# Performance work log

Measured on AMD Instinct MI355X. Metric: run time of the kernel, lower is better.

The kernel has to match this reference:

```python
import jax, jax.numpy as jnp
import numpy as np

D_MODEL = 1024
N_HEADS = 16
D_HEAD = D_MODEL // N_HEADS
B, L = 4, 2048
NEG_INF = float('-inf')


def setup_inputs() -> dict:
    key = jax.random.key(0)
    ks = jax.random.split(key, 8)
    x = jax.random.normal(ks[0], (B, L, D_MODEL), dtype=jnp.float32)
    # sorted cumulative event times in hours (~0-2000h span)
    timestamps = jnp.cumsum(jax.random.uniform(ks[1], (B, L), dtype=jnp.float32), axis=-1)
    mask = jnp.ones((B, L), dtype=jnp.float32)
    s = 1.0 / np.sqrt(D_MODEL)
    W_qkv = jax.random.normal(ks[2], (3 * D_MODEL, D_MODEL), dtype=jnp.float32) * s
    b_qkv = jnp.zeros((3 * D_MODEL,), dtype=jnp.float32)
    W_out = jax.random.normal(ks[3], (D_MODEL, D_MODEL), dtype=jnp.float32) * s
    b_out = jnp.zeros((D_MODEL,), dtype=jnp.float32)
    decay_rate = jnp.full((N_HEADS,), 0.01, dtype=jnp.float32)
    return {"x": x, "timestamps": timestamps, "mask": mask,
            "W_qkv": W_qkv, "b_qkv": b_qkv, "W_out": W_out, "b_out": b_out,
            "decay_rate": decay_rate}


def reference(x, timestamps, mask, W_qkv, b_qkv, W_out, b_out, decay_rate):
    Bb, Ll, Dd = x.shape
    H, dh = N_HEADS, D_HEAD
    scale = dh ** (-0.5)
    qkv = x @ W_qkv.T + b_qkv                     # (B,L,3D)
    qkv = qkv.reshape(Bb, Ll, 3, H, dh).transpose(2, 0, 3, 1, 4)  # (3,B,H,L,dh)
    q, k, v = qkv[0], qkv[1], qkv[2]
    attn = jnp.einsum('bhqd,bhkd->bhqk', q, k) * scale
    t_diff = jnp.abs(timestamps[:, :, None] - timestamps[:, None, :])[:, None]  # (B,1,L,L)
    decay = jax.nn.softplus(decay_rate)[None, :, None, None]                    # (1,H,1,1)
    attn = attn - decay * t_diff / 24.0
    causal = jnp.triu(jnp.ones((Ll, Ll), dtype=bool), k=1)        # (L,L) True above diag
    attn = jnp.where(causal[None, None], NEG_INF, attn)
    pad = (mask == 0.0)[:, None, None, :]                         # (B,1,1,L) True=pad key
    attn = jnp.where(pad, NEG_INF, attn)
    attn = jax.nn.softmax(attn, axis=-1)
    out = jnp.einsum('bhqk,bhkd->bhqd', attn, v)                  # (B,H,L,dh)
    out = out.transpose(0, 2, 1, 3).reshape(Bb, Ll, Dd)
    return out @ W_out.T + b_out
```

## Files before the change

kernel.cpp:

```cpp
#include <hip/hip_runtime.h>
#include <stdint.h>
#include <math.h>

#define B_   4
#define L_   2048
#define H_   16
#define DH_  64
#define DM_  1024

typedef __bf16 bf16;
typedef __attribute__((ext_vector_type(8))) __bf16 bf16x8;
typedef __attribute__((ext_vector_type(4))) float f32x4;
typedef __attribute__((ext_vector_type(4))) int i32x4;
typedef __attribute__((ext_vector_type(4))) short s16x4;
typedef unsigned short u16;
typedef unsigned int u32;
typedef __attribute__((ext_vector_type(2))) unsigned int u32x2;
typedef __attribute__((ext_vector_type(4))) unsigned short u16x4;

typedef unsigned int u32g __attribute__((address_space(1)));
typedef unsigned int u32l __attribute__((address_space(3)));

__device__ __forceinline__ u16 f2bf(float f) {
  return __builtin_bit_cast(u16, (bf16)f);
}

__device__ __forceinline__ float exp2_fast(float x) {
  float r; asm("v_exp_f32 %0, %1" : "=v"(r) : "v"(x)); return r;
}

__device__ __forceinline__ void gload16(const void* g, void* l) {
  __builtin_amdgcn_global_load_lds((const u32g*)g, (u32l*)l, 16, 0, 0);
}

__device__ __forceinline__ f32x4 mfma16(s16x4 a, s16x4 b, f32x4 c) {
#if __has_builtin(__builtin_amdgcn_mfma_f32_16x16x16bf16_1k)
  return __builtin_amdgcn_mfma_f32_16x16x16bf16_1k(a, b, c, 0, 0, 0);
#else
  asm volatile("v_mfma_f32_16x16x16_bf16 %0, %1, %2, %0\n\ts_nop 7\n\ts_nop 2"
               : "+v"(c) : "v"(a), "v"(b));
  return c;
#endif
}

#define NX4 2097152
#define NQ4 786432
#define NO4 262144
#define NTOT4 (NX4 + NQ4 + NO4)
__global__ __launch_bounds__(256) void cvt3b(const float* __restrict__ x,
                                             const float* __restrict__ wq,
                                             const float* __restrict__ wo,
                                             u16* __restrict__ xb, u16* __restrict__ wqb,
                                             u16* __restrict__ wob,
                                             const float* __restrict__ ts,
                                             const float* __restrict__ msk,
                                             const float* __restrict__ decay,
                                             float* __restrict__ Bk) {
  int i = blockIdx.x * 256 + threadIdx.x;
  if (i >= NTOT4) {
    int j = i - NTOT4;
    int bh = j >> 11, l = j & (L_ - 1);
    int b = bh >> 4, h = bh & 15;
    float dc24 = log1pf(__expf(decay[h])) * (1.0f / 24.0f) * 1.44269504f;
    float tv = ts[b * L_ + l], mv = msk[b * L_ + l];
    Bk[j] = (mv != 0.f) ? dc24 * tv : -INFINITY;
    return;
  }
  const float* src; u16* dst; int j;
  if (i < NX4)            { src = x;  dst = xb;  j = i; }
  else if (i < NX4 + NQ4) { src = wq; dst = wqb; j = i - NX4; }
  else                    { src = wo; dst = wob; j = i - NX4 - NQ4; }
  f32x4 v = ((const f32x4*)src)[j];
  u16x4 o;
  o[0] = f2bf(v[0]); o[1] = f2bf(v[1]); o[2] = f2bf(v[2]); o[3] = f2bf(v[3]);
  ((u16x4*)dst)[j] = o;
}

__global__ __launch_bounds__(512) void gemm_qkv(
    const u16* __restrict__ A, const u16* __restrict__ Bm, const float* __restrict__ bias,
    u16* __restrict__ Qb, u16* __restrict__ Kb, u16* __restrict__ Vt)
{
  __shared__ char smem[135168];
  u16* ltr = (u16*)smem;
  const int K = 1024, nk = 16;

  const int tid = threadIdx.x;
  const int nwg = gridDim.x;
  int idx = blockIdx.x;
  idx = (idx & 7) * (nwg >> 3) + (idx >> 3);
  const int nbx = 12;
  const int bx = idx % nbx, by = idx / nbx;
  const int m0 = by << 8, n0 = bx << 8;

  const int lane = tid & 63, w = tid >> 6;
  const int g = lane >> 4, col = lane & 15;
  const int wr = w >> 2, wc = w & 3;

  f32x4 acc[8][4];
#pragma unroll
  for (int mt = 0; mt < 8; ++mt)
#pragma unroll
    for (int nt = 0; nt < 4; ++nt) {
      acc[mt][nt][0] = 0.f; acc[mt][nt][1] = 0.f;
      acc[mt][nt][2] = 0.f; acc[mt][nt][3] = 0.f;
    }

  auto SA = [&](int kt, int nb, int q) {
    char* dA = smem + (nb << 16);
    int c = (q << 9) + tid;
    int row = c >> 3, cc = c & 7;
    gload16(A + (size_t)(m0 + row) * K + (kt << 6) + ((cc ^ (row & 7)) << 3), dA + c * 16);
  };
  auto SB = [&](int kt, int nb, int q) {
    char* dB = smem + (nb << 16) + 32768;
    int c = (q << 9) + tid;
    int row = c >> 3, cc = c & 7;
    gload16(Bm + (size_t)(n0 + row) * K + (kt << 6) + ((cc ^ (row & 7)) << 3), dB + c * 16);
  };

  SA(0, 0, 0); SA(0, 0, 1); SA(0, 0, 2); SA(0, 0, 3);
  SB(0, 0, 0); SB(0, 0, 1); SB(0, 0, 2); SB(0, 0, 3);
  SA(1, 1, 0); SA(1, 1, 2); SB(1, 1, 0); SB(1, 1, 1); SA(1, 1, 1); SA(1, 1, 3);
  asm volatile("s_waitcnt vmcnt(6)" ::: "memory");
  __builtin_amdgcn_s_barrier();

  for (int t = 0; t < nk; ++t) {
    const char* bufA = smem + ((t & 1) << 16);
    const char* bufB = bufA + 32768;
    const int nbN = (t + 1) & 1;

    auto RDA = [&](int mt, int kk) {
      int row = wr * 128 + mt * 16 + col;
      return *(const bf16x8*)(bufA + row * 128 + ((((kk << 2) + g) ^ (row & 7)) << 4));
    };
    auto RDB = [&](int nt, int kk) {
      int row = wc * 64 + nt * 16 + col;
      return *(const bf16x8*)(bufB + row * 128 + ((((kk << 2) + g) ^ (row & 7)) << 4));
    };

    bf16x8 af[4][2], bfr[4][2];

#pragma unroll
    for (int mi = 0; mi < 4; ++mi) { af[mi][0] = RDA(mi, 0); af[mi][1] = RDA(mi, 1); }
#pragma unroll
    for (int ni = 0; ni < 2; ++ni) { bfr[ni][0] = RDB(ni, 0); bfr[ni][1] = RDB(ni, 1); }
    if (t + 1 < nk) { SB(t + 1, nbN, 2); SB(t + 1, nbN, 3); }
    __builtin_amdgcn_s_barrier();
    asm volatile("s_waitcnt lgkmcnt(0)" ::: "memory");
    __builtin_amdgcn_sched_barrier(0);
    __builtin_amdgcn_s_setprio(1);
#pragma unroll
    for (int mi = 0; mi < 4; ++mi)
#pragma unroll
      for (int ni = 0; ni < 2; ++ni)
#pragma unroll
        for (int kk = 0; kk < 2; ++kk)
          acc[mi][ni] = __builtin_amdgcn_mfma_f32_16x16x32_bf16(af[mi][kk], bfr[ni][kk], acc[mi][ni], 0, 0, 0);
    __builtin_amdgcn_s_setprio(0);
    __builtin_amdgcn_s_barrier();

#pragma unroll
    for (int ni = 2; ni < 4; ++ni) { bfr[ni][0] = RDB(ni, 0); bfr[ni][1] = RDB(ni, 1); }
    if (t + 2 < nk) { SA(t + 2, t & 1, 0); SA(t + 2, t & 1, 2); }
    __builtin_amdgcn_s_barrier();
    asm volatile("s_waitcnt lgkmcnt(0)" ::: "memory");
    __builtin_amdgcn_sched_barrier(0);
    __builtin_amdgcn_s_setprio(1);
#pragma unroll
    for (int mi = 0; mi < 4; ++mi)
#pragma unroll
      for (int ni = 2; ni < 4; ++ni)
#pragma unroll
        for (int kk = 0; kk < 2; ++kk)
          acc[mi][ni] = __builtin_amdgcn_mfma_f32_16x16x32_bf16(af[mi][kk], bfr[ni][kk], acc[mi][ni], 0, 0, 0);
    __builtin_amdgcn_s_setprio(0);
    __builtin_amdgcn_s_barrier();

#pragma unroll
    for (int mi = 0; mi < 4; ++mi) { af[mi][0] = RDA(mi + 4, 0); af[mi][1] = RDA(mi + 4, 1); }
    if (t + 2 < nk) { SB(t + 2, t & 1, 0); SB(t + 2, t & 1, 1); }
    __builtin_amdgcn_s_barrier();
    asm volatile("s_waitcnt lgkmcnt(0)" ::: "memory");
    __builtin_amdgcn_sched_barrier(0);
    __builtin_amdgcn_s_setprio(1);
#pragma unroll
    for (int mi = 0; mi < 4; ++mi)
#pragma unroll
      for (int ni = 2; ni < 4; ++ni)
#pragma unroll
        for (int kk = 0; kk < 2; ++kk)
          acc[mi + 4][ni] = __builtin_amdgcn_mfma_f32_16x16x32_bf16(af[mi][kk], bfr[ni][kk], acc[mi + 4][ni], 0, 0, 0);
    __builtin_amdgcn_s_setprio(0);
    __builtin_amdgcn_s_barrier();

    if (t + 2 < nk) { SA(t + 2, t & 1, 1); SA(t + 2, t & 1, 3); }
    __builtin_amdgcn_s_setprio(1);
#pragma unroll
    for (int mi = 0; mi < 4; ++mi)
#pragma unroll
      for (int ni = 0; ni < 2; ++ni)
#pragma unroll
        for (int kk = 0; kk < 2; ++kk)
          acc[mi + 4][ni] = __builtin_amdgcn_mfma_f32_16x16x32_bf16(af[mi][kk], bfr[ni][kk], acc[mi + 4][ni], 0, 0, 0);
    __builtin_amdgcn_s_setprio(0);
    if (t + 2 < nk) asm volatile("s_waitcnt vmcnt(6)" ::: "memory");
    else            asm volatile("s_waitcnt vmcnt(0)" ::: "memory");
    __builtin_amdgcn_s_barrier();
  }

  const int type = n0 >> 10;
  const float qsc = (type == 0) ? 0.125f * 1.44269504f : 1.0f;
#pragma unroll
  for (int nt = 0; nt < 4; ++nt) {
    int nn = wc * 64 + nt * 16 + col;
    float bv = bias[n0 + nn];
#pragma unroll
    for (int mt = 0; mt < 8; ++mt) {
      int mm = wr * 128 + mt * 16 + g * 4;
#pragma unroll
      for (int r = 0; r < 4; ++r) {
        u16 hv = f2bf((acc[mt][nt][r] + bv) * qsc);
        if (type < 2) ltr[(mm + r) * 264 + nn] = hv;
        else          ltr[nn * 264 + (mm + r)] = hv;
      }
    }
  }
  __syncthreads();
  if (type < 2) {
#pragma unroll
    for (int it = 0; it < 16; ++it) {
      int cid = tid + it * 512;
      int rrow = cid >> 5, cc = cid & 31;
      i32x4 v = *(const i32x4*)((const char*)ltr + rrow * 528 + cc * 16);
      int token = m0 + rrow;
      int bb = token >> 11, ll = token & (L_ - 1);
      int gn = n0 + cc * 8;
      int head = (gn & 1023) >> 6, d = gn & 63;
      u16* dst = (type == 0) ? Qb : Kb;
      *(i32x4*)(dst + ((size_t)((bb * H_ + head) * L_ + ll)) * 64 + d) = v;
    }
  } else {
#pragma unroll
    for (int it = 0; it < 16; ++it) {
      int cid = tid + it * 512;
      int rrow = cid >> 5, cc = cid & 31;
      i32x4 v = *(const i32x4*)((const char*)ltr + rrow * 528 + cc * 16);
      int gn = n0 + rrow;
      int head = (gn & 1023) >> 6, d = gn & 63;
      int token0 = m0 + cc * 8;
      int bb = token0 >> 11, ll = token0 & (L_ - 1);
      *(i32x4*)(Vt + ((size_t)((bb * H_ + head) * DH_ + d)) * L_ + ll) = v;
    }
  }
}

__global__ __launch_bounds__(512) void gemm_bf16(
    const u16* __restrict__ A, const u16* __restrict__ Bm, const float* __restrict__ bias,
    int M, int N, int K, int mode,
    u16* __restrict__ Qb, u16* __restrict__ Kb, u16* __restrict__ Vt, float* __restrict__ Cout)
{
  __shared__ char smem[147456];
  const int tid = threadIdx.x;
  const int nwg = gridDim.x;
  int idx = blockIdx.x;
  idx = (idx & 7) * (nwg >> 3) + (idx >> 3);
  const int nbx = N >> 7;
  const int bx = idx % nbx, by = idx / nbx;
  const int m0 = by << 8, n0 = bx << 7;

  const int lane = tid & 63, w = tid >> 6;
  const int g = lane >> 4, col = lane & 15;
  const int wr = w >> 1, wc = w & 1;

  f32x4 acc[4][4];
#pragma unroll
  for (int mt = 0; mt < 4; ++mt)
#pragma unroll
    for (int nt = 0; nt < 4; ++nt) {
      acc[mt][nt][0] = 0.f; acc[mt][nt][1] = 0.f;
      acc[mt][nt][2] = 0.f; acc[mt][nt][3] = 0.f;
    }

  auto STAGE_A = [&](int kt, int nb, int hh) {
    char* dA = smem + nb * 49152;
    const int k0 = kt << 6;
#pragma unroll
    for (int pp = hh * 2; pp < hh * 2 + 2; ++pp) {
      int c = tid + pp * 512;
      int row = c >> 3, cc = c & 7;
      gload16(A + (size_t)(m0 + row) * K + k0 + ((cc ^ (row & 7)) << 3), dA + c * 16);
    }
  };
  auto STAGE_B = [&](int kt, int nb) {
    char* dB = smem + nb * 49152 + 32768;
    const int k0 = kt << 6;
#pragma unroll
    for (int pp = 0; pp < 2; ++pp) {
      int c = tid + pp * 512;
      int row = c >> 3, cc = c & 7;
      gload16(Bm + (size_t)(n0 + row) * K + k0 + ((cc ^ (row & 7)) << 3), dB + c * 16);
    }
  };

  STAGE_A(0, 0, 0); STAGE_A(0, 0, 1); STAGE_B(0, 0);
  STAGE_A(1, 1, 0); STAGE_A(1, 1, 1); STAGE_B(1, 1);
  asm volatile("s_waitcnt vmcnt(6)" ::: "memory");
  __builtin_amdgcn_s_barrier();

  const int nk = K >> 6;
  for (int t = 0; t < nk; ++t) {
    const char* bufA = smem + (t % 3) * 49152;
    const char* bufB = bufA + 32768;
    const bool pf = (t + 2 < nk);
    const int nb2 = (t + 2) % 3;

    bf16x8 af[4][2], bfr[4][2];
    auto RDA = [&](int mt, int kk) {
      int row = wr * 64 + mt * 16 + col;
      return *(const bf16x8*)(bufA + row * 128 + ((((kk << 2) + g) ^ (row & 7)) << 4));
    };
    auto RDB = [&](int nt, int kk) {
      int row = wc * 64 + nt * 16 + col;
      return *(const bf16x8*)(bufB + row * 128 + ((((kk << 2) + g) ^ (row & 7)) << 4));
    };
    auto QUAD = [&](int qm, int qn) {
      __builtin_amdgcn_s_setprio(1);
#pragma unroll
      for (int mi = 0; mi < 2; ++mi)
#pragma unroll
        for (int ni = 0; ni < 2; ++ni)
#pragma unroll
          for (int kk = 0; kk < 2; ++kk)
            acc[qm * 2 + mi][qn * 2 + ni] = __builtin_amdgcn_mfma_f32_16x16x32_bf16(
                af[qm * 2 + mi][kk], bfr[qn * 2 + ni][kk], acc[qm * 2 + mi][qn * 2 + ni], 0, 0, 0);
      __builtin_amdgcn_s_setprio(0);
    };

#pragma unroll
    for (int mi = 0; mi < 2; ++mi) { af[mi][0] = RDA(mi, 0); af[mi][1] = RDA(mi, 1); }
#pragma unroll
    for (int ni = 0; ni < 2; ++ni) { bfr[ni][0] = RDB(ni, 0); bfr[ni][1] = RDB(ni, 1); }
    if (pf) STAGE_A(t + 2, nb2, 0);
    __builtin_amdgcn_s_barrier();
    asm volatile("s_waitcnt lgkmcnt(0)" ::: "memory");
    __builtin_amdgcn_sched_barrier(0);
    QUAD(0, 0);
    __builtin_amdgcn_s_barrier();

#pragma unroll
    for (int ni = 2; ni < 4; ++ni) { bfr[ni][0] = RDB(ni, 0); bfr[ni][1] = RDB(ni, 1); }
    if (pf) STAGE_A(t + 2, nb2, 1);
    __builtin_amdgcn_s_barrier();
    asm volatile("s_waitcnt lgkmcnt(0)" ::: "memory");
    __builtin_amdgcn_sched_barrier(0);
    QUAD(0, 1);
    __builtin_amdgcn_s_barrier();

#pragma unroll
    for (int mi = 2; mi < 4; ++mi) { af[mi][0] = RDA(mi, 0); af[mi][1] = RDA(mi, 1); }
    if (pf) STAGE_B(t + 2, nb2);
    __builtin_amdgcn_s_barrier();
    asm volatile("s_waitcnt lgkmcnt(0)" ::: "memory");
    __builtin_amdgcn_sched_barrier(0);
    QUAD(1, 1);
    __builtin_amdgcn_s_barrier();

    QUAD(1, 0);
    if (pf)              asm volatile("s_waitcnt vmcnt(6)" ::: "memory");
    else if (t + 1 < nk) asm volatile("s_waitcnt vmcnt(0)" ::: "memory");
    __builtin_amdgcn_s_barrier();
  }

#pragma unroll
  for (int nt = 0; nt < 4; ++nt) {
    int gn = n0 + wc * 64 + nt * 16 + col;
    float bv = bias[gn];
#pragma unroll
    for (int mt = 0; mt < 4; ++mt) {
      int mbase = m0 + wr * 64 + mt * 16 + g * 4;
#pragma unroll
      for (int r = 0; r < 4; ++r)
        Cout[(size_t)(mbase + r) * N + gn] = acc[mt][nt][r] + bv;
    }
  }
}

__global__ __launch_bounds__(512, 2) void attn_fwd(
    const u16* __restrict__ Qb, const u16* __restrict__ Kb, const u16* __restrict__ Vt,
    const float* __restrict__ Bk, u16* __restrict__ AO)
{
  __shared__ u16 lK[3][64 * 64];
  __shared__ u16 lV[3][64 * 64];

  const int phys = blockIdx.x;
  const int xcd = phys & 7, s = phys >> 3;
  const int bh = xcd * 8 + (s >> 3);
  const int pr = s & 7;
  const int qa = pr, qbt = 15 - pr;
  const int b = bh >> 4, h = bh & 15;

  const int tid = threadIdx.x, w = tid >> 6, lane = tid & 63;
  const int g = lane >> 4, q16 = lane & 15;

  const float* Bkb = Bk + (size_t)bh * L_;

  int kcol[2], vcol[4];
#pragma unroll
  for (int kk = 0; kk < 2; ++kk) kcol[kk] = ((kk * 4 + g) ^ (q16 & 7)) << 4;
#pragma unroll
  for (int t = 0; t < 4; ++t)
    vcol[t] = (((2 * t + (g >> 1)) ^ (q16 & 7)) << 4) + (g & 1) * 8;

  const int nkA = (qa + 1) * 2;
  const int nkB = (qbt + 1) * 2;

  auto STAGE = [&](int gst, int nb) {
    const int kt = (gst < nkA) ? gst : gst - nkA;
    const int kg0 = kt * 64;
    const int r8 = tid >> 3, cc = tid & 7;
    gload16(Kb + ((size_t)bh * L_ + kg0 + r8) * 64 + ((cc ^ (r8 & 7)) * 8),
            (char*)lK[nb] + tid * 16);
    gload16(Vt + ((size_t)(bh * 64 + r8)) * L_ + kg0 + ((cc ^ (r8 & 7)) * 8),
            (char*)lV[nb] + tid * 16);
  };

  auto QKBODY = [&](bf16x8 (&qf)[2], float& l_r, float mn,
                    int qrow, int kg0, int cur, s16x4 (&pf)[4]) {
    f32x4 sv[4];
#pragma unroll
    for (int t = 0; t < 4; ++t)
      sv[t] = *(const f32x4*)(Bkb + kg0 + t * 16 + g * 4);

    __builtin_amdgcn_s_setprio(1);
#pragma unroll
    for (int t = 0; t < 4; ++t) {
      const char* krow = (const char*)lK[cur] + t * 2048 + q16 * 128;
#pragma unroll
      for (int kk = 0; kk < 2; ++kk) {
        bf16x8 kf = *(const bf16x8*)(krow + kcol[kk]);
        sv[t] = __builtin_amdgcn_mfma_f32_16x16x32_bf16(kf, qf[kk], sv[t], 0, 0, 0);
      }
    }
    __builtin_amdgcn_s_setprio(0);

    if (kg0 + 63 > qrow) {
      const int qg = qrow + q16;
#pragma unroll
      for (int t = 0; t < 4; ++t)
#pragma unroll
        for (int r = 0; r < 4; ++r)
          sv[t][r] = (kg0 + t * 16 + g * 4 + r <= qg) ? sv[t][r] : -INFINITY;
    }

    float rs = 0.f;
#pragma unroll
    for (int t = 0; t < 4; ++t) {
      s16x4 pp;
#pragma unroll
      for (int r = 0; r < 4; ++r) {
        float pv = exp2_fast(sv[t][r] - mn);
        rs += pv;
        pp[r] = (short)f2bf(pv);
      }
      pf[t] = pp;
    }
    l_r += rs;
  };

  auto PVBODY = [&](f32x4 (&o)[4], s16x4 (&pf)[4], int vb) {
    __builtin_amdgcn_s_setprio(1);
#pragma unroll
    for (int t = 0; t < 4; ++t) {
      const char* vrow = (const char*)lV[vb] + q16 * 128 + vcol[t];
#pragma unroll
      for (int db = 0; db < 4; ++db) {
        s16x4 vf = *(const s16x4*)(vrow + db * 2048);
        o[db] = mfma16(vf, pf[t], o[db]);
      }
    }
    __builtin_amdgcn_s_setprio(0);
  };

  auto EPI = [&](f32x4 (&o)[4], float l_r, int qt) {
    float lt = l_r + __shfl_xor(l_r, 16);
    lt += __shfl_xor(lt, 32);
    float inv = 1.f / lt;
    u16* dst = AO + ((size_t)(b * L_ + qt * 128 + w * 16 + q16)) * DM_ + h * 64 + g * 4;
#pragma unroll
    for (int db = 0; db < 4; ++db) {
      u32x2 pk;
      pk[0] = (u32)f2bf(o[db][0] * inv) | ((u32)f2bf(o[db][1] * inv) << 16);
      pk[1] = (u32)f2bf(o[db][2] * inv) | ((u32)f2bf(o[db][3] * inv) << 16);
      *(u32x2*)(dst + db * 16) = pk;
    }
  };

  STAGE(0, 0);
  asm volatile("s_waitcnt vmcnt(0) lgkmcnt(0)" ::: "memory");
  __builtin_amdgcn_s_barrier();
  __builtin_amdgcn_sched_barrier(0);

  {
    const int qrow = qa * 128 + w * 16;
    const int mkt = (qrow + 79) >> 6;
    const float mn = Bkb[qrow + q16] + 8.f;
    bf16x8 qf[2];
    {
      const u16* Qr = Qb + ((size_t)bh * L_ + qrow + q16) * 64;
      qf[0] = *(const bf16x8*)(Qr + g * 8);
      qf[1] = *(const bf16x8*)(Qr + 32 + g * 8);
    }
    float l_r = 0.f;
    f32x4 o[4];
#pragma unroll
    for (int db = 0; db < 4; ++db) {
      o[db][0] = 0.f; o[db][1] = 0.f; o[db][2] = 0.f; o[db][3] = 0.f;
    }
    s16x4 pfP[4];
    int pvb = 0;
    bool pvalid = false;
    for (int st = 0; st < nkA; ++st) {
      const int cur = st % 3;
      STAGE(st + 1, (st + 1) % 3);
      const bool doqk = st < mkt;
      s16x4 pfC[4];
      if (doqk) QKBODY(qf, l_r, mn, qrow, st * 64, cur, pfC);
      if (pvalid) PVBODY(o, pfP, pvb);
      if (doqk) {
#pragma unroll
        for (int t = 0; t < 4; ++t) pfP[t] = pfC[t];
        pvb = cur;
      }
      pvalid = doqk;
      asm volatile("s_waitcnt vmcnt(0) lgkmcnt(0)" ::: "memory");
      __builtin_amdgcn_s_barrier();
      __builtin_amdgcn_sched_barrier(0);
    }
    if (pvalid) PVBODY(o, pfP, pvb);
    EPI(o, l_r, qa);
  }
  __builtin_amdgcn_s_barrier();

  {
    const int qrow = qbt * 128 + w * 16;
    const int mkt = (qrow + 79) >> 6;
    const float mn = Bkb[qrow + q16] + 8.f;
    bf16x8 qf[2];
    {
      const u16* Qr = Qb + ((size_t)bh * L_ + qrow + q16) * 64;
      qf[0] = *(const bf16x8*)(Qr + g * 8);
      qf[1] = *(const bf16x8*)(Qr + 32 + g * 8);
    }
    float l_r = 0.f;
    f32x4 o[4];
#pragma unroll
    for (int db = 0; db < 4; ++db) {
      o[db][0] = 0.f; o[db][1] = 0.f; o[db][2] = 0.f; o[db][3] = 0.f;
    }
    s16x4 pfP[4];
    int pvb = 0;
    bool pvalid = false;
    for (int kt = 0; kt < nkB; ++kt) {
      const int gst = nkA + kt;
      const int cur = gst % 3;
      if (kt + 1 < nkB) STAGE(gst + 1, (gst + 1) % 3);
      const bool doqk = kt < mkt;
      s16x4 pfC[4];
      if (doqk) QKBODY(qf, l_r, mn, qrow, kt * 64, cur, pfC);
      if (pvalid) PVBODY(o, pfP, pvb);
      if (doqk) {
#pragma unroll
        for (int t = 0; t < 4; ++t) pfP[t] = pfC[t];
        pvb = cur;
      }
      pvalid = doqk;
      if (kt + 1 < nkB) {
        asm volatile("s_waitcnt vmcnt(0) lgkmcnt(0)" ::: "memory");
        __builtin_amdgcn_s_barrier();
        __builtin_amdgcn_sched_barrier(0);
      }
    }
    if (pvalid) PVBODY(o, pfP, pvb);
    EPI(o, l_r, qbt);
  }
}

extern "C" void kernel_launch(void* const* d_in, const int* in_sizes, int n_in,
                              void* d_out, int out_size, void* d_ws, size_t ws_size,
                              hipStream_t stream) {
  const float* x    = (const float*)d_in[0];
  const float* ts   = (const float*)d_in[1];
  const float* mk   = (const float*)d_in[2];
  const float* Wqkv = (const float*)d_in[3];
  const float* bqkv = (const float*)d_in[4];
  const float* Wout = (const float*)d_in[5];
  const float* bout = (const float*)d_in[6];
  const float* dec  = (const float*)d_in[7];
  float* out = (float*)d_out;

  char* ws = (char*)d_ws;
  u16* xbf  = (u16*)(ws + 0);
  u16* wqbf = (u16*)(ws + 16777216);
  u16* wobf = (u16*)(ws + 23068672);
  u16* Qb   = (u16*)(ws + 25165824);
  u16* Kb   = (u16*)(ws + 41943040);
  u16* Vt   = (u16*)(ws + 58720256);
  u16* AO   = (u16*)(ws + 75497472);
  float* Bk = (float*)(ws + 92274688);

  cvt3b<<<dim3((NTOT4 + 64 * 2048) / 256), 256, 0, stream>>>(
      x, Wqkv, Wout, xbf, wqbf, wobf, ts, mk, dec, Bk);

  gemm_qkv<<<dim3(384), 512, 0, stream>>>(xbf, wqbf, bqkv, Qb, Kb, Vt);

  attn_fwd<<<dim3(512), 512, 0, stream>>>(Qb, Kb, Vt, Bk, AO);

  gemm_bf16<<<dim3(256), 512, 0, stream>>>(
      AO, wobf, bout, 8192, 1024, 1024, 1, nullptr, nullptr, nullptr, out);
}
```

Before: 171.6 us.

## Software-pipeline LDS fragment reads across GEMM k-tiles with ping-pong registers

Restructures the QKV projection GEMM main loop so that LDS reads of A/B fragments for each MFMA phase are issued before the preceding MFMA block. The next tile's first A and B fragments are prefetched at the end of the current tile. The loop is unrolled by two with ping-pong B register sets, and the vmcnt wait is moved earlier. The goal is to hide LDS read latency behind MFMA work and drop some barriers, at the cost of more live VGPRs and the assumption that nk is even.

```diff
diff --git a/kernel.cpp b/kernel.cpp
--- a/kernel.cpp
+++ b/kernel.cpp
@@ -118,36 +118,58 @@
     gload16(Bm + (size_t)(n0 + row) * K + (kt << 6) + ((cc ^ (row & 7)) << 3), dB + c * 16);
   };
 
+  auto RDA = [&](const char* bA, int mt, int kk) {
+    int row = wr * 128 + mt * 16 + col;
+    return *(const bf16x8*)(bA + row * 128 + ((((kk << 2) + g) ^ (row & 7)) << 4));
+  };
+  auto RDB = [&](const char* bB, int nt, int kk) {
+    int row = wc * 64 + nt * 16 + col;
+    return *(const bf16x8*)(bB + row * 128 + ((((kk << 2) + g) ^ (row & 7)) << 4));
+  };
+
+  bf16x8 afA[4][2], afB[4][2], bfX[2][2], bfY[2][2];
+
   SA(0, 0, 0); SA(0, 0, 1); SA(0, 0, 2); SA(0, 0, 3);
   SB(0, 0, 0); SB(0, 0, 1); SB(0, 0, 2); SB(0, 0, 3);
   SA(1, 1, 0); SA(1, 1, 2); SB(1, 1, 0); SB(1, 1, 1); SA(1, 1, 1); SA(1, 1, 3);
   asm volatile("s_waitcnt vmcnt(6)" ::: "memory");
   __builtin_amdgcn_s_barrier();
-
-  for (int t = 0; t < nk; ++t) {
+#pragma unroll
+  for (int mi = 0; mi < 4; ++mi) { afA[mi][0] = RDA(smem, mi, 0); afA[mi][1] = RDA(smem, mi, 1); }
+#pragma unroll
+  for (int ni = 0; ni < 2; ++ni) { bfX[ni][0] = RDB(smem + 32768, ni, 0); bfX[ni][1] = RDB(smem + 32768, ni, 1); }
+
+  auto TILE = [&](int t, bf16x8 (&LO)[2][2], bf16x8 (&HI)[2][2]) {
     const char* bufA = smem + ((t & 1) << 16);
     const char* bufB = bufA + 32768;
+    const char* bufAn = smem + (((t + 1) & 1) << 16);
+    const char* bufBn = bufAn + 32768;
     const int nbN = (t + 1) & 1;
-
-    auto RDA = [&](int mt, int kk) {
-      int row = wr * 128 + mt * 16 + col;
-      return *(const bf16x8*)(bufA + row * 128 + ((((kk << 2) + g) ^ (row & 7)) << 4));
-    };
-    auto RDB = [&](int nt, int kk) {
-      int row = wc * 64 + nt * 16 + col;
-      return *(const bf16x8*)(bufB + row * 128 + ((((kk << 2) + g) ^ (row & 7)) << 4));
-    };
-
-    bf16x8 af[4][2], bfr[4][2];
-
-#pragma unroll
-    for (int mi = 0; mi < 4; ++mi) { af[mi][0] = RDA(mi, 0); af[mi][1] = RDA(mi, 1); }
-#pragma unroll
-    for (int ni = 0; ni < 2; ++ni) { bfr[ni][0] = RDB(ni, 0); bfr[ni][1] = RDB(ni, 1); }
+    const int nbC = t & 1;
+
+    asm volatile("s_waitcnt lgkmcnt(0)" ::: "memory");
+    __builtin_amdgcn_sched_barrier(0);
+#pragma unroll
+    for (int ni = 0; ni < 2; ++ni) { HI[ni][0] = RDB(bufB, ni + 2, 0); HI[ni][1] = RDB(bufB, ni + 2, 1); }
     if (t + 1 < nk) { SB(t + 1, nbN, 2); SB(t + 1, nbN, 3); }
-    __builtin_amdgcn_s_barrier();
+    __builtin_amdgcn_sched_barrier(0);
+    __builtin_amdgcn_s_setprio(1);
+#pragma unroll
+    for (int mi = 0; mi < 4; ++mi)
+#pragma unroll
+      for (int ni = 0; ni < 2; ++ni)
+#pragma unroll
+        for (int kk = 0; kk < 2; ++kk)
+          acc[mi][ni] = __builtin_amdgcn_mfma_f32_16x16x32_bf16(afA[mi][kk], LO[ni][kk], acc[mi][ni], 0, 0, 0);
+    __builtin_amdgcn_s_setprio(0);
+    __builtin_amdgcn_s_barrier();
+
     asm volatile("s_waitcnt lgkmcnt(0)" ::: "memory");
     __builtin_amdgcn_sched_barrier(0);
+#pragma unroll
+    for (int mi = 0; mi < 4; ++mi) { afB[mi][0] = RDA(bufA, mi + 4, 0); afB[mi][1] = RDA(bufA, mi + 4, 1); }
+    if (t + 2 < nk) { SA(t + 2, nbC, 0); SA(t + 2, nbC, 2); }
+    __builtin_amdgcn_sched_barrier(0);
     __builtin_amdgcn_s_setprio(1);
 #pragma unroll
     for (int mi = 0; mi < 4; ++mi)
@@ -155,57 +177,51 @@
       for (int ni = 0; ni < 2; ++ni)
 #pragma unroll
         for (int kk = 0; kk < 2; ++kk)
-          acc[mi][ni] = __builtin_amdgcn_mfma_f32_16x16x32_bf16(af[mi][kk], bfr[ni][kk], acc[mi][ni], 0, 0, 0);
+          acc[mi][ni + 2] = __builtin_amdgcn_mfma_f32_16x16x32_bf16(afA[mi][kk], HI[ni][kk], acc[mi][ni + 2], 0, 0, 0);
     __builtin_amdgcn_s_setprio(0);
     __builtin_amdgcn_s_barrier();
 
-#pragma unroll
-    for (int ni = 2; ni < 4; ++ni) { bfr[ni][0] = RDB(ni, 0); bfr[ni][1] = RDB(ni, 1); }
-    if (t + 2 < nk) { SA(t + 2, t & 1, 0); SA(t + 2, t & 1, 2); }
-    __builtin_amdgcn_s_barrier();
     asm volatile("s_waitcnt lgkmcnt(0)" ::: "memory");
     __builtin_amdgcn_sched_barrier(0);
+    if (t + 2 < nk) { SB(t + 2, nbC, 0); SB(t + 2, nbC, 1); }
+    __builtin_amdgcn_sched_barrier(0);
     __builtin_amdgcn_s_setprio(1);
 #pragma unroll
     for (int mi = 0; mi < 4; ++mi)
 #pragma unroll
-      for (int ni = 2; ni < 4; ++ni)
+      for (int ni = 0; ni < 2; ++ni)
 #pragma unroll
         for (int kk = 0; kk < 2; ++kk)
-          acc[mi][ni] = __builtin_amdgcn_mfma_f32_16x16x32_bf16(af[mi][kk], bfr[ni][kk], acc[mi][ni], 0, 0, 0);
+          acc[mi + 4][ni + 2] = __builtin_amdgcn_mfma_f32_16x16x32_bf16(afB[mi][kk], HI[ni][kk], acc[mi + 4][ni + 2], 0, 0, 0);
     __builtin_amdgcn_s_setprio(0);
-    __builtin_amdgcn_s_barrier();
-
-#pragma unroll
-    for (int mi = 0; mi < 4; ++mi) { af[mi][0] = RDA(mi + 4, 0); af[mi][1] = RDA(mi + 4, 1); }
-    if (t + 2 < nk) { SB(t + 2, t & 1, 0); SB(t + 2, t & 1, 1); }
-    __builtin_amdgcn_s_barrier();
-    asm volatile("s_waitcnt lgkmcnt(0)" ::: "memory");
+    if (t + 2 < nk) asm volatile("s_waitcnt vmcnt(4)" ::: "memory");
+    else            asm volatile("s_waitcnt vmcnt(0)" ::: "memory");
+    __builtin_amdgcn_s_barrier();
+
+    __builtin_amdgcn_sched_barrier(0);
+    if (t + 1 < nk) {
+#pragma unroll
+      for (int mi = 0; mi < 4; ++mi) { afA[mi][0] = RDA(bufAn, mi, 0); afA[mi][1] = RDA(bufAn, mi, 1); }
+#pragma unroll
+      for (int ni = 0; ni < 2; ++ni) { HI[ni][0] = RDB(bufBn, ni, 0); HI[ni][1] = RDB(bufBn, ni, 1); }
+    }
+    if (t + 2 < nk) { SA(t + 2, nbC, 1); SA(t + 2, nbC, 3); }
     __builtin_amdgcn_sched_barrier(0);
     __builtin_amdgcn_s_setprio(1);
 #pragma unroll
     for (int mi = 0; mi < 4; ++mi)
 #pragma unroll
-      for (int ni = 2; ni < 4; ++ni)
+      for (int ni = 0; ni < 2; ++ni)
 #pragma unroll
         for (int kk = 0; kk < 2; ++kk)
-          acc[mi + 4][ni] = __builtin_amdgcn_mfma_f32_16x16x32_bf16(af[mi][kk], bfr[ni][kk], acc[mi + 4][ni], 0, 0, 0);
+          acc[mi + 4][ni] = __builtin_amdgcn_mfma_f32_16x16x32_bf16(afB[mi][kk], LO[ni][kk], acc[mi + 4][ni], 0, 0, 0);
     __builtin_amdgcn_s_setprio(0);
     __builtin_amdgcn_s_barrier();
-
-    if (t + 2 < nk) { SA(t + 2, t & 1, 1); SA(t + 2, t & 1, 3); }
-    __builtin_amdgcn_s_setprio(1);
-#pragma unroll
-    for (int mi = 0; mi < 4; ++mi)
-#pragma unroll
-      for (int ni = 0; ni < 2; ++ni)
-#pragma unroll
-        for (int kk = 0; kk < 2; ++kk)
-          acc[mi + 4][ni] = __builtin_amdgcn_mfma_f32_16x16x32_bf16(af[mi][kk], bfr[ni][kk], acc[mi + 4][ni], 0, 0, 0);
-    __builtin_amdgcn_s_setprio(0);
-    if (t + 2 < nk) asm volatile("s_waitcnt vmcnt(6)" ::: "memory");
-    else            asm volatile("s_waitcnt vmcnt(0)" ::: "memory");
-    __builtin_amdgcn_s_barrier();
+  };
+
+  for (int t = 0; t < nk; t += 2) {
+    TILE(t, bfX, bfY);
+    TILE(t + 1, bfY, bfX);
   }
 
   const int type = n0 >> 10;
```

Result: slower. 246.2 us (+43.5%).

## Load GEMM B operand directly from global into registers, bypassing LDS

Applied to the files above, without the earlier changes.

The QKV projection GEMM no longer stages the B (weight) tile through shared memory. Each wave now loads its B fragments straight from global memory into two register banks, ping-ponging across the four MFMA phases with adjusted vmcnt waits. LDS drops to only the double-buffered A tile, which removes LDS write and read traffic for B and frees shared memory. The cost is uncoalesced, redundant global loads of B across waves sharing a column tile, extra register pressure, and more exposed global-memory latency.

```diff
diff --git a/kernel.cpp b/kernel.cpp
--- a/kernel.cpp
+++ b/kernel.cpp
@@ -106,47 +106,45 @@
     }
 
   auto SA = [&](int kt, int nb, int q) {
-    char* dA = smem + (nb << 16);
+    char* dA = smem + (nb << 15);
     int c = (q << 9) + tid;
     int row = c >> 3, cc = c & 7;
     gload16(A + (size_t)(m0 + row) * K + (kt << 6) + ((cc ^ (row & 7)) << 3), dA + c * 16);
   };
-  auto SB = [&](int kt, int nb, int q) {
-    char* dB = smem + (nb << 16) + 32768;
-    int c = (q << 9) + tid;
-    int row = c >> 3, cc = c & 7;
-    gload16(Bm + (size_t)(n0 + row) * K + (kt << 6) + ((cc ^ (row & 7)) << 3), dB + c * 16);
+
+  auto RDA = [&](const char* bA, int mt, int kk) {
+    int row = wr * 128 + mt * 16 + col;
+    return *(const bf16x8*)(bA + row * 128 + ((((kk << 2) + g) ^ (row & 7)) << 4));
+  };
+
+  bf16x8 af[4][2], bfrA[2][2], bfrB[2][2];
+
+  auto LDB = [&](bf16x8 (&bank)[2][2], int kt, int half) {
+    const int k0 = kt << 6;
+#pragma unroll
+    for (int n2 = 0; n2 < 2; ++n2)
+#pragma unroll
+      for (int kk = 0; kk < 2; ++kk) {
+        int row = wc * 64 + (half * 2 + n2) * 16 + col;
+        bank[n2][kk] = *(const bf16x8*)(Bm + (size_t)(n0 + row) * K + k0 + (((kk << 2) + g) << 3));
+      }
   };
 
   SA(0, 0, 0); SA(0, 0, 1); SA(0, 0, 2); SA(0, 0, 3);
-  SB(0, 0, 0); SB(0, 0, 1); SB(0, 0, 2); SB(0, 0, 3);
-  SA(1, 1, 0); SA(1, 1, 2); SB(1, 1, 0); SB(1, 1, 1); SA(1, 1, 1); SA(1, 1, 3);
-  asm volatile("s_waitcnt vmcnt(6)" ::: "memory");
+  LDB(bfrA, 0, 0);
+  SA(1, 1, 0); SA(1, 1, 1); SA(1, 1, 2); SA(1, 1, 3);
+  asm volatile("s_waitcnt vmcnt(4)" ::: "memory");
   __builtin_amdgcn_s_barrier();
 
   for (int t = 0; t < nk; ++t) {
-    const char* bufA = smem + ((t & 1) << 16);
-    const char* bufB = bufA + 32768;
-    const int nbN = (t + 1) & 1;
-
-    auto RDA = [&](int mt, int kk) {
-      int row = wr * 128 + mt * 16 + col;
-      return *(const bf16x8*)(bufA + row * 128 + ((((kk << 2) + g) ^ (row & 7)) << 4));
-    };
-    auto RDB = [&](int nt, int kk) {
-      int row = wc * 64 + nt * 16 + col;
-      return *(const bf16x8*)(bufB + row * 128 + ((((kk << 2) + g) ^ (row & 7)) << 4));
-    };
-
-    bf16x8 af[4][2], bfr[4][2];
-
-#pragma unroll
-    for (int mi = 0; mi < 4; ++mi) { af[mi][0] = RDA(mi, 0); af[mi][1] = RDA(mi, 1); }
-#pragma unroll
-    for (int ni = 0; ni < 2; ++ni) { bfr[ni][0] = RDB(ni, 0); bfr[ni][1] = RDB(ni, 1); }
-    if (t + 1 < nk) { SB(t + 1, nbN, 2); SB(t + 1, nbN, 3); }
-    __builtin_amdgcn_s_barrier();
-    asm volatile("s_waitcnt lgkmcnt(0)" ::: "memory");
+    const char* bufA = smem + ((t & 1) << 15);
+    const int nbC = t & 1;
+
+#pragma unroll
+    for (int mi = 0; mi < 4; ++mi) { af[mi][0] = RDA(bufA, mi, 0); af[mi][1] = RDA(bufA, mi, 1); }
+    LDB(bfrB, t, 1);
+    __builtin_amdgcn_s_barrier();
+    asm volatile("s_waitcnt vmcnt(4) lgkmcnt(0)" ::: "memory");
     __builtin_amdgcn_sched_barrier(0);
     __builtin_amdgcn_s_setprio(1);
 #pragma unroll
@@ -155,45 +153,50 @@
       for (int ni = 0; ni < 2; ++ni)
 #pragma unroll
         for (int kk = 0; kk < 2; ++kk)
-          acc[mi][ni] = __builtin_amdgcn_mfma_f32_16x16x32_bf16(af[mi][kk], bfr[ni][kk], acc[mi][ni], 0, 0, 0);
+          acc[mi][ni] = __builtin_amdgcn_mfma_f32_16x16x32_bf16(af[mi][kk], bfrA[ni][kk], acc[mi][ni], 0, 0, 0);
     __builtin_amdgcn_s_setprio(0);
     __builtin_amdgcn_s_barrier();
 
-#pragma unroll
-    for (int ni = 2; ni < 4; ++ni) { bfr[ni][0] = RDB(ni, 0); bfr[ni][1] = RDB(ni, 1); }
-    if (t + 2 < nk) { SA(t + 2, t & 1, 0); SA(t + 2, t & 1, 2); }
-    __builtin_amdgcn_s_barrier();
-    asm volatile("s_waitcnt lgkmcnt(0)" ::: "memory");
+    LDB(bfrA, t, 1);
+    if (t + 2 < nk) { SA(t + 2, nbC, 0); SA(t + 2, nbC, 2); }
+    __builtin_amdgcn_s_barrier();
+    if (t + 2 < nk) asm volatile("s_waitcnt vmcnt(6)" ::: "memory");
+    else            asm volatile("s_waitcnt vmcnt(4)" ::: "memory");
     __builtin_amdgcn_sched_barrier(0);
     __builtin_amdgcn_s_setprio(1);
 #pragma unroll
     for (int mi = 0; mi < 4; ++mi)
 #pragma unroll
-      for (int ni = 2; ni < 4; ++ni)
+      for (int ni = 0; ni < 2; ++ni)
 #pragma unroll
         for (int kk = 0; kk < 2; ++kk)
-          acc[mi][ni] = __builtin_amdgcn_mfma_f32_16x16x32_bf16(af[mi][kk], bfr[ni][kk], acc[mi][ni], 0, 0, 0);
+          acc[mi][ni + 2] = __builtin_amdgcn_mfma_f32_16x16x32_bf16(af[mi][kk], bfrB[ni][kk], acc[mi][ni + 2], 0, 0, 0);
     __builtin_amdgcn_s_setprio(0);
     __builtin_amdgcn_s_barrier();
 
 #pragma unroll
-    for (int mi = 0; mi < 4; ++mi) { af[mi][0] = RDA(mi + 4, 0); af[mi][1] = RDA(mi + 4, 1); }
-    if (t + 2 < nk) { SB(t + 2, t & 1, 0); SB(t + 2, t & 1, 1); }
-    __builtin_amdgcn_s_barrier();
-    asm volatile("s_waitcnt lgkmcnt(0)" ::: "memory");
+    for (int mi = 0; mi < 4; ++mi) { af[mi][0] = RDA(bufA, mi + 4, 0); af[mi][1] = RDA(bufA, mi + 4, 1); }
+    LDB(bfrB, t, 0);
+    __builtin_amdgcn_s_barrier();
+    asm volatile("s_waitcnt vmcnt(4) lgkmcnt(0)" ::: "memory");
     __builtin_amdgcn_sched_barrier(0);
     __builtin_amdgcn_s_setprio(1);
 #pragma unroll
     for (int mi = 0; mi < 4; ++mi)
 #pragma unroll
-      for (int ni = 2; ni < 4; ++ni)
+      for (int ni = 0; ni < 2; ++ni)
 #pragma unroll
         for (int kk = 0; kk < 2; ++kk)
-          acc[mi + 4][ni] = __builtin_amdgcn_mfma_f32_16x16x32_bf16(af[mi][kk], bfr[ni][kk], acc[mi + 4][ni], 0, 0, 0);
+          acc[mi + 4][ni + 2] = __builtin_amdgcn_mfma_f32_16x16x32_bf16(af[mi][kk], bfrA[ni][kk], acc[mi + 4][ni + 2], 0, 0, 0);
     __builtin_amdgcn_s_setprio(0);
     __builtin_amdgcn_s_barrier();
 
-    if (t + 2 < nk) { SA(t + 2, t & 1, 1); SA(t + 2, t & 1, 3); }
+    if (t + 1 < nk) LDB(bfrA, t + 1, 0);
+    if (t + 2 < nk) { SA(t + 2, nbC, 1); SA(t + 2, nbC, 3); }
+    if (t + 2 < nk)      asm volatile("s_waitcnt vmcnt(6)" ::: "memory");
+    else if (t + 1 < nk) asm volatile("s_waitcnt vmcnt(4)" ::: "memory");
+    else                 asm volatile("s_waitcnt vmcnt(0)" ::: "memory");
+    __builtin_amdgcn_sched_barrier(0);
     __builtin_amdgcn_s_setprio(1);
 #pragma unroll
     for (int mi = 0; mi < 4; ++mi)
@@ -201,10 +204,8 @@
       for (int ni = 0; ni < 2; ++ni)
 #pragma unroll
         for (int kk = 0; kk < 2; ++kk)
-          acc[mi + 4][ni] = __builtin_amdgcn_mfma_f32_16x16x32_bf16(af[mi][kk], bfr[ni][kk], acc[mi + 4][ni], 0, 0, 0);
+          acc[mi + 4][ni] = __builtin_amdgcn_mfma_f32_16x16x32_bf16(af[mi][kk], bfrB[ni][kk], acc[mi + 4][ni], 0, 0, 0);
     __builtin_amdgcn_s_setprio(0);
-    if (t + 2 < nk) asm volatile("s_waitcnt vmcnt(6)" ::: "memory");
-    else            asm volatile("s_waitcnt vmcnt(0)" ::: "memory");
     __builtin_amdgcn_s_barrier();
   }
 
```

New measurement: 236.6 us. 37.8% more time.

## Retile QKV GEMM to 256x192 tiles for 512 workgroups

Applied to the files above, without the earlier changes.

Changes the QKV projection GEMM tile from 256x256 to 256x192, so the grid grows from 384 to 512 workgroups and fills the 256 CUs in two even waves instead of leaving a partial second wave. The B-buffer staging, pipeline load schedule and vmcnt waits are reworked for three 64-row B chunks per k-step. Tiles that straddle the K/V boundary go through a split epilogue with separate row-major and transposed LDS staging. Each workgroup now reuses A less per tile, and the epilogue gains more branches.

```diff
diff --git a/kernel.cpp b/kernel.cpp
--- a/kernel.cpp
+++ b/kernel.cpp
@@ -80,7 +80,7 @@
     const u16* __restrict__ A, const u16* __restrict__ Bm, const float* __restrict__ bias,
     u16* __restrict__ Qb, u16* __restrict__ Kb, u16* __restrict__ Vt)
 {
-  __shared__ char smem[135168];
+  __shared__ char smem[114688];
   u16* ltr = (u16*)smem;
   const int K = 1024, nk = 16;
 
@@ -88,63 +88,65 @@
   const int nwg = gridDim.x;
   int idx = blockIdx.x;
   idx = (idx & 7) * (nwg >> 3) + (idx >> 3);
-  const int nbx = 12;
+  const int nbx = 16;
   const int bx = idx % nbx, by = idx / nbx;
-  const int m0 = by << 8, n0 = bx << 8;
+  const int m0 = by << 8, n0 = bx * 192;
 
   const int lane = tid & 63, w = tid >> 6;
   const int g = lane >> 4, col = lane & 15;
   const int wr = w >> 2, wc = w & 3;
 
-  f32x4 acc[8][4];
+  f32x4 acc[8][3];
 #pragma unroll
   for (int mt = 0; mt < 8; ++mt)
 #pragma unroll
-    for (int nt = 0; nt < 4; ++nt) {
+    for (int nt = 0; nt < 3; ++nt) {
       acc[mt][nt][0] = 0.f; acc[mt][nt][1] = 0.f;
       acc[mt][nt][2] = 0.f; acc[mt][nt][3] = 0.f;
     }
 
   auto SA = [&](int kt, int nb, int q) {
-    char* dA = smem + (nb << 16);
+    char* dA = smem + nb * 32768;
     int c = (q << 9) + tid;
     int row = c >> 3, cc = c & 7;
     gload16(A + (size_t)(m0 + row) * K + (kt << 6) + ((cc ^ (row & 7)) << 3), dA + c * 16);
   };
   auto SB = [&](int kt, int nb, int q) {
-    char* dB = smem + (nb << 16) + 32768;
+    char* dB = smem + 65536 + nb * 24576;
     int c = (q << 9) + tid;
     int row = c >> 3, cc = c & 7;
     gload16(Bm + (size_t)(n0 + row) * K + (kt << 6) + ((cc ^ (row & 7)) << 3), dB + c * 16);
   };
 
+  auto RDA = [&](const char* bA, int mt, int kk) {
+    int row = wr * 128 + mt * 16 + col;
+    return *(const bf16x8*)(bA + row * 128 + ((((kk << 2) + g) ^ (row & 7)) << 4));
+  };
+  auto RDB = [&](const char* bB, int nt, int kk) {
+    int row = wc * 48 + nt * 16 + col;
+    return *(const bf16x8*)(bB + row * 128 + ((((kk << 2) + g) ^ (row & 7)) << 4));
+  };
+
   SA(0, 0, 0); SA(0, 0, 1); SA(0, 0, 2); SA(0, 0, 3);
-  SB(0, 0, 0); SB(0, 0, 1); SB(0, 0, 2); SB(0, 0, 3);
-  SA(1, 1, 0); SA(1, 1, 2); SB(1, 1, 0); SB(1, 1, 1); SA(1, 1, 1); SA(1, 1, 3);
-  asm volatile("s_waitcnt vmcnt(6)" ::: "memory");
+  SB(0, 0, 0); SB(0, 0, 1); SB(0, 0, 2);
+  SA(1, 1, 0); SA(1, 1, 1); SA(1, 1, 2); SA(1, 1, 3);
+  SB(1, 1, 0);
+  asm volatile("s_waitcnt vmcnt(5)" ::: "memory");
   __builtin_amdgcn_s_barrier();
 
   for (int t = 0; t < nk; ++t) {
-    const char* bufA = smem + ((t & 1) << 16);
-    const char* bufB = bufA + 32768;
+    const char* bufA = smem + (t & 1) * 32768;
+    const char* bufB = smem + 65536 + (t & 1) * 24576;
     const int nbN = (t + 1) & 1;
-
-    auto RDA = [&](int mt, int kk) {
-      int row = wr * 128 + mt * 16 + col;
-      return *(const bf16x8*)(bufA + row * 128 + ((((kk << 2) + g) ^ (row & 7)) << 4));
-    };
-    auto RDB = [&](int nt, int kk) {
-      int row = wc * 64 + nt * 16 + col;
-      return *(const bf16x8*)(bufB + row * 128 + ((((kk << 2) + g) ^ (row & 7)) << 4));
-    };
-
-    bf16x8 af[4][2], bfr[4][2];
-
-#pragma unroll
-    for (int mi = 0; mi < 4; ++mi) { af[mi][0] = RDA(mi, 0); af[mi][1] = RDA(mi, 1); }
-#pragma unroll
-    for (int ni = 0; ni < 2; ++ni) { bfr[ni][0] = RDB(ni, 0); bfr[ni][1] = RDB(ni, 1); }
-    if (t + 1 < nk) { SB(t + 1, nbN, 2); SB(t + 1, nbN, 3); }
+    const int nbC = t & 1;
+
+    bf16x8 af[4][2], bf[3][2];
+
+#pragma unroll
+    for (int mi = 0; mi < 4; ++mi) { af[mi][0] = RDA(bufA, mi, 0); af[mi][1] = RDA(bufA, mi, 1); }
+#pragma unroll
+    for (int ni = 0; ni < 2; ++ni) { bf[ni][0] = RDB(bufB, ni, 0); bf[ni][1] = RDB(bufB, ni, 1); }
+    if (t + 1 < nk) { SB(t + 1, nbN, 1); SB(t + 1, nbN, 2); }
     __builtin_amdgcn_s_barrier();
     asm volatile("s_waitcnt lgkmcnt(0)" ::: "memory");
     __builtin_amdgcn_sched_barrier(0);
@@ -155,13 +157,12 @@
       for (int ni = 0; ni < 2; ++ni)
 #pragma unroll
         for (int kk = 0; kk < 2; ++kk)
-          acc[mi][ni] = __builtin_amdgcn_mfma_f32_16x16x32_bf16(af[mi][kk], bfr[ni][kk], acc[mi][ni], 0, 0, 0);
+          acc[mi][ni] = __builtin_amdgcn_mfma_f32_16x16x32_bf16(af[mi][kk], bf[ni][kk], acc[mi][ni], 0, 0, 0);
     __builtin_amdgcn_s_setprio(0);
     __builtin_amdgcn_s_barrier();
 
-#pragma unroll
-    for (int ni = 2; ni < 4; ++ni) { bfr[ni][0] = RDB(ni, 0); bfr[ni][1] = RDB(ni, 1); }
-    if (t + 2 < nk) { SA(t + 2, t & 1, 0); SA(t + 2, t & 1, 2); }
+    bf[2][0] = RDB(bufB, 2, 0); bf[2][1] = RDB(bufB, 2, 1);
+    if (t + 2 < nk) { SA(t + 2, nbC, 0); SA(t + 2, nbC, 2); }
     __builtin_amdgcn_s_barrier();
     asm volatile("s_waitcnt lgkmcnt(0)" ::: "memory");
     __builtin_amdgcn_sched_barrier(0);
@@ -169,16 +170,14 @@
 #pragma unroll
     for (int mi = 0; mi < 4; ++mi)
 #pragma unroll
-      for (int ni = 2; ni < 4; ++ni)
-#pragma unroll
-        for (int kk = 0; kk < 2; ++kk)
-          acc[mi][ni] = __builtin_amdgcn_mfma_f32_16x16x32_bf16(af[mi][kk], bfr[ni][kk], acc[mi][ni], 0, 0, 0);
+      for (int kk = 0; kk < 2; ++kk)
+        acc[mi][2] = __builtin_amdgcn_mfma_f32_16x16x32_bf16(af[mi][kk], bf[2][kk], acc[mi][2], 0, 0, 0);
     __builtin_amdgcn_s_setprio(0);
     __builtin_amdgcn_s_barrier();
 
 #pragma unroll
-    for (int mi = 0; mi < 4; ++mi) { af[mi][0] = RDA(mi + 4, 0); af[mi][1] = RDA(mi + 4, 1); }
-    if (t + 2 < nk) { SB(t + 2, t & 1, 0); SB(t + 2, t & 1, 1); }
+    for (int mi = 0; mi < 4; ++mi) { af[mi][0] = RDA(bufA, mi + 4, 0); af[mi][1] = RDA(bufA, mi + 4, 1); }
+    if (t + 2 < nk) SB(t + 2, nbC, 0);
     __builtin_amdgcn_s_barrier();
     asm volatile("s_waitcnt lgkmcnt(0)" ::: "memory");
     __builtin_amdgcn_sched_barrier(0);
@@ -186,70 +185,90 @@
 #pragma unroll
     for (int mi = 0; mi < 4; ++mi)
 #pragma unroll
-      for (int ni = 2; ni < 4; ++ni)
+      for (int kk = 0; kk < 2; ++kk)
+        acc[mi + 4][2] = __builtin_amdgcn_mfma_f32_16x16x32_bf16(af[mi][kk], bf[2][kk], acc[mi + 4][2], 0, 0, 0);
+    __builtin_amdgcn_s_setprio(0);
+    __builtin_amdgcn_s_barrier();
+
+    if (t + 2 < nk) { SA(t + 2, nbC, 1); SA(t + 2, nbC, 3); }
+    __builtin_amdgcn_s_setprio(1);
+#pragma unroll
+    for (int mi = 0; mi < 4; ++mi)
+#pragma unroll
+      for (int ni = 0; ni < 2; ++ni)
 #pragma unroll
         for (int kk = 0; kk < 2; ++kk)
-          acc[mi + 4][ni] = __builtin_amdgcn_mfma_f32_16x16x32_bf16(af[mi][kk], bfr[ni][kk], acc[mi + 4][ni], 0, 0, 0);
+          acc[mi + 4][ni] = __builtin_amdgcn_mfma_f32_16x16x32_bf16(af[mi][kk], bf[ni][kk], acc[mi + 4][ni], 0, 0, 0);
     __builtin_amdgcn_s_setprio(0);
-    __builtin_amdgcn_s_barrier();
-
-    if (t + 2 < nk) { SA(t + 2, t & 1, 1); SA(t + 2, t & 1, 3); }
-    __builtin_amdgcn_s_setprio(1);
-#pragma unroll
-    for (int mi = 0; mi < 4; ++mi)
-#pragma unroll
-      for (int ni = 0; ni < 2; ++ni)
-#pragma unroll
-        for (int kk = 0; kk < 2; ++kk)
-          acc[mi + 4][ni] = __builtin_amdgcn_mfma_f32_16x16x32_bf16(af[mi][kk], bfr[ni][kk], acc[mi + 4][ni], 0, 0, 0);
-    __builtin_amdgcn_s_setprio(0);
-    if (t + 2 < nk) asm volatile("s_waitcnt vmcnt(6)" ::: "memory");
+    if (t + 2 < nk) asm volatile("s_waitcnt vmcnt(5)" ::: "memory");
     else            asm volatile("s_waitcnt vmcnt(0)" ::: "memory");
     __builtin_amdgcn_s_barrier();
   }
 
-  const int type = n0 >> 10;
-  const float qsc = (type == 0) ? 0.125f * 1.44269504f : 1.0f;
-#pragma unroll
-  for (int nt = 0; nt < 4; ++nt) {
-    int nn = wc * 64 + nt * 16 + col;
-    float bv = bias[n0 + nn];
-#pragma unroll
-    for (int mt = 0; mt < 8; ++mt) {
-      int mm = wr * 128 + mt * 16 + g * 4;
-#pragma unroll
-      for (int r = 0; r < 4; ++r) {
-        u16 hv = f2bf((acc[mt][nt][r] + bv) * qsc);
-        if (type < 2) ltr[(mm + r) * 264 + nn] = hv;
-        else          ltr[nn * 264 + (mm + r)] = hv;
-      }
-    }
-  }
-  __syncthreads();
-  if (type < 2) {
-#pragma unroll
-    for (int it = 0; it < 16; ++it) {
+  const float QSC = 0.125f * 1.44269504f;
+  if (n0 < 2048) {
+#pragma unroll
+    for (int nt = 0; nt < 3; ++nt) {
+      int nn = wc * 48 + nt * 16 + col;
+      int gn = n0 + nn;
+      if (gn < 2048) {
+        float bv = bias[gn];
+        float sc = (gn < 1024) ? QSC : 1.0f;
+#pragma unroll
+        for (int mt = 0; mt < 8; ++mt) {
+          int mm = wr * 128 + mt * 16 + g * 4;
+#pragma unroll
+          for (int r = 0; r < 4; ++r)
+            ltr[(mm + r) * 200 + nn] = f2bf((acc[mt][nt][r] + bv) * sc);
+        }
+      }
+    }
+    __syncthreads();
+#pragma unroll
+    for (int it = 0; it < 12; ++it) {
+      int cid = tid + it * 512;
+      int rrow = cid / 24, cc = cid % 24;
+      int gn = n0 + cc * 8;
+      if (gn < 2048) {
+        i32x4 v = *(const i32x4*)((const char*)ltr + rrow * 400 + cc * 16);
+        int token = m0 + rrow;
+        int bb = token >> 11, ll = token & (L_ - 1);
+        int head = (gn & 1023) >> 6, d = gn & 63;
+        u16* dst = (gn < 1024) ? Qb : Kb;
+        *(i32x4*)(dst + ((size_t)((bb * H_ + head) * L_ + ll)) * 64 + d) = v;
+      }
+    }
+  }
+  if (n0 + 191 >= 2048) {
+    __syncthreads();
+#pragma unroll
+    for (int nt = 0; nt < 3; ++nt) {
+      int nn = wc * 48 + nt * 16 + col;
+      int gn = n0 + nn;
+      if (gn >= 2048) {
+        float bv = bias[gn];
+#pragma unroll
+        for (int mt = 0; mt < 8; ++mt) {
+          int mm = wr * 128 + mt * 16 + g * 4;
+#pragma unroll
+          for (int r = 0; r < 4; ++r)
+            ltr[nn * 264 + (mm + r)] = f2bf(acc[mt][nt][r] + bv);
+        }
+      }
+    }
+    __syncthreads();
+#pragma unroll
+    for (int it = 0; it < 12; ++it) {
       int cid = tid + it * 512;
       int rrow = cid >> 5, cc = cid & 31;
-      i32x4 v = *(const i32x4*)((const char*)ltr + rrow * 528 + cc * 16);
-      int token = m0 + rrow;
-      int bb = token >> 11, ll = token & (L_ - 1);
-      int gn = n0 + cc * 8;
-      int head = (gn & 1023) >> 6, d = gn & 63;
-      u16* dst = (type == 0) ? Qb : Kb;
-      *(i32x4*)(dst + ((size_t)((bb * H_ + head) * L_ + ll)) * 64 + d) = v;
-    }
-  } else {
-#pragma unroll
-    for (int it = 0; it < 16; ++it) {
-      int cid = tid + it * 512;
-      int rrow = cid >> 5, cc = cid & 31;
-      i32x4 v = *(const i32x4*)((const char*)ltr + rrow * 528 + cc * 16);
       int gn = n0 + rrow;
-      int head = (gn & 1023) >> 6, d = gn & 63;
-      int token0 = m0 + cc * 8;
-      int bb = token0 >> 11, ll = token0 & (L_ - 1);
-      *(i32x4*)(Vt + ((size_t)((bb * H_ + head) * DH_ + d)) * L_ + ll) = v;
+      if (gn >= 2048) {
+        i32x4 v = *(const i32x4*)((const char*)ltr + rrow * 528 + cc * 16);
+        int head = (gn & 1023) >> 6, d = gn & 63;
+        int token0 = m0 + cc * 8;
+        int bb = token0 >> 11, ll = token0 & (L_ - 1);
+        *(i32x4*)(Vt + ((size_t)((bb * H_ + head) * DH_ + d)) * L_ + ll) = v;
+      }
     }
   }
 }
@@ -611,7 +630,7 @@
   cvt3b<<<dim3((NTOT4 + 64 * 2048) / 256), 256, 0, stream>>>(
       x, Wqkv, Wout, xbf, wqbf, wobf, ts, mk, dec, Bk);
 
-  gemm_qkv<<<dim3(384), 512, 0, stream>>>(xbf, wqbf, bqkv, Qb, Kb, Vt);
+  gemm_qkv<<<dim3(512), 512, 0, stream>>>(xbf, wqbf, bqkv, Qb, Kb, Vt);
 
   attn_fwd<<<dim3(512), 512, 0, stream>>>(Qb, Kb, Vt, Bk, AO);
 
```

Result: faster. 167.3 us (-2.5%).
